# Performance work log

Hardware: AMD Instinct MI355X
Metric: run time of the kernel (lower is better)

The kernel has to match this reference:

```python
import jax, jax.numpy as jnp
import numpy as np

N, E = 65536, 524288
IN_DIM, HID_DIM, OUT_DIM = 1024, 512, 256


def setup_inputs() -> dict:
    key = jax.random.key(0)
    k1, k2, k3, k4, k5, k6 = jax.random.split(key, 6)
    h = jax.random.normal(k1, (N, IN_DIM), dtype=jnp.float32)
    src = jax.random.randint(k2, (E,), 0, N, dtype=jnp.int64)
    dst = jax.random.randint(k3, (E,), 0, N, dtype=jnp.int64)
    # Glorot-uniform weights as in DGL GraphConv
    lim1 = float(np.sqrt(6.0 / (IN_DIM + HID_DIM)))
    lim2 = float(np.sqrt(6.0 / (HID_DIM + OUT_DIM)))
    W1 = jax.random.uniform(k4, (IN_DIM, HID_DIM), jnp.float32, -lim1, lim1)
    W2 = jax.random.uniform(k5, (HID_DIM, OUT_DIM), jnp.float32, -lim2, lim2)
    b1 = jnp.zeros((HID_DIM,), jnp.float32)
    b2 = jnp.zeros((OUT_DIM,), jnp.float32)
    return {"h": h, "W1": W1, "b1": b1, "W2": W2, "b2": b2, "src": src, "dst": dst}


def _graph_conv(x, W, b, src, dst, inv_sqrt_dout, inv_sqrt_din):
    # DGL GraphConv, norm='both': D_in^{-1/2} A D_out^{-1/2} X W + b
    # Apply dense transform first (in_dim >= out_dim path in DGL) -- same math.
    x = x * inv_sqrt_dout[:, None]
    x = x @ W  # [N, out]
    agg = jax.ops.segment_sum(x[src], dst, num_segments=x.shape[0])  # scatter-add over edges
    return agg * inv_sqrt_din[:, None] + b


def reference(h, W1, b1, W2, b2, src, dst):
    n = h.shape[0]
    ones = jnp.ones((src.shape[0],), h.dtype)
    deg_out = jnp.maximum(jax.ops.segment_sum(ones, src, num_segments=n), 1.0)
    deg_in = jnp.maximum(jax.ops.segment_sum(ones, dst, num_segments=n), 1.0)
    inv_sqrt_dout = jax.lax.rsqrt(deg_out)
    inv_sqrt_din = jax.lax.rsqrt(deg_in)
    x = _graph_conv(h, W1, b1, src, dst, inv_sqrt_dout, inv_sqrt_din)
    x = jax.nn.elu(x)  # act; dropout p=0 -> identity
    out = _graph_conv(x, W2, b2, src, dst, inv_sqrt_dout, inv_sqrt_din)
    return out  # last_act = Identity
```

## Files before the change

kernel.cpp:

```cpp
#include <hip/hip_runtime.h>
#include <hip/hip_bf16.h>

#define IN_DIM 1024
#define HID 512
#define OUTD 256

typedef __attribute__((ext_vector_type(8))) short short8;
typedef __attribute__((ext_vector_type(4))) float f32x4;
typedef __attribute__((ext_vector_type(8))) unsigned short ushort8e;
typedef __attribute__((ext_vector_type(4))) unsigned int uint4e;


__device__ inline unsigned short f2bf(float f) {
    union { float f; unsigned u; } v; v.f = f;
    unsigned r = (v.u + 0x7FFF + ((v.u >> 16) & 1)) >> 16;
    return (unsigned short)r;
}

__device__ inline float bf2f(unsigned short u) {
    union { unsigned u; float f; } v; v.u = ((unsigned)u) << 16; return v.f;
}

__device__ inline unsigned pk2(float a, float b) {
    unsigned ua = __float_as_uint(a) + 0x8000u;
    unsigned ub = __float_as_uint(b) + 0x8000u;
#if __has_builtin(__builtin_amdgcn_perm)
    return __builtin_amdgcn_perm(ub, ua, 0x07060302u);
#else
    return (ua >> 16) | (ub & 0xFFFF0000u);
#endif
}

__device__ inline void gload16(const void* g, void* l) {
    __builtin_amdgcn_global_load_lds(
        (const __attribute__((address_space(1))) void*)g,
        (__attribute__((address_space(3))) void*)l, 16, 0, 0);
}


__global__ void deg_kernel(const int* __restrict__ src, const int* __restrict__ dst,
                           int* __restrict__ dego, int* __restrict__ degi, int E) {
    int i = blockIdx.x * blockDim.x + threadIdx.x;
    if (i < E) {
        atomicAdd(&dego[src[i]], 1);
        atomicAdd(&degi[dst[i]], 1);
    }
}

__global__ void invsqrt_kernel(const int* __restrict__ dego, const int* __restrict__ degi,
                               float* __restrict__ iso, float* __restrict__ isi, int n) {
    int i = blockIdx.x * blockDim.x + threadIdx.x;
    if (i < n) {
        iso[i] = rsqrtf(fmaxf((float)dego[i], 1.0f));
        isi[i] = rsqrtf(fmaxf((float)degi[i], 1.0f));
    }
}


__global__ __launch_bounds__(256) void scan_block(const int* __restrict__ deg,
                                                  int* __restrict__ excl,
                                                  int* __restrict__ partials) {
    __shared__ int tmp[256];
    int tid = threadIdx.x;
    int i = blockIdx.x * 256 + tid;
    int v = deg[i];
    tmp[tid] = v;
    __syncthreads();
    #pragma unroll
    for (int off = 1; off < 256; off <<= 1) {
        int t = (tid >= off) ? tmp[tid - off] : 0;
        __syncthreads();
        tmp[tid] += t;
        __syncthreads();
    }
    excl[i] = tmp[tid] - v;
    if (tid == 255) partials[blockIdx.x] = tmp[255];
}

__global__ __launch_bounds__(256) void scan_partials(int* __restrict__ partials) {
    __shared__ int tmp[256];
    int tid = threadIdx.x;
    int v = partials[tid];
    tmp[tid] = v;
    __syncthreads();
    #pragma unroll
    for (int off = 1; off < 256; off <<= 1) {
        int t = (tid >= off) ? tmp[tid - off] : 0;
        __syncthreads();
        tmp[tid] += t;
        __syncthreads();
    }
    partials[tid] = tmp[tid] - v;
}

__global__ __launch_bounds__(256) void scan_add(const int* __restrict__ excl,
                                                const int* __restrict__ partials,
                                                const int* __restrict__ deg,
                                                int* __restrict__ row_start,
                                                int* __restrict__ cursor, int n) {
    int i = blockIdx.x * 256 + threadIdx.x;
    int v = excl[i] + partials[blockIdx.x];
    row_start[i] = v;
    cursor[i] = v;
    if (i == n - 1) row_start[n] = v + deg[i];
}

__global__ void csr_fill(const int* __restrict__ src, const int* __restrict__ dst,
                         int* __restrict__ cursor, int* __restrict__ eidx, int E) {
    int e = blockIdx.x * blockDim.x + threadIdx.x;
    if (e < E) {
        int pos = atomicAdd(&cursor[dst[e]], 1);
        eidx[pos] = src[e];
    }
}


__global__ __launch_bounds__(256) void transpose_cvt_tiled(
    const float* __restrict__ W, unsigned short* __restrict__ Wt, int K, int N)
{
    __shared__ unsigned short tile[32][33];
    const int tx = threadIdx.x & 31;
    const int ty = threadIdx.x >> 5;
    const int n0 = blockIdx.x * 32;
    const int k0 = blockIdx.y * 32;

    #pragma unroll
    for (int j = 0; j < 4; ++j) {
        int k = ty + j * 8;
        tile[k][tx] = f2bf(W[(size_t)(k0 + k) * N + n0 + tx]);
    }
    __syncthreads();
    #pragma unroll
    for (int j = 0; j < 4; ++j) {
        int n = ty + j * 8;
        Wt[(size_t)(n0 + n) * K + k0 + tx] = tile[tx][n];
    }
}


#define NXCD 8

__global__ __launch_bounds__(256, 4) void gemm1_f32lds(
    const float* __restrict__ A, const unsigned short* __restrict__ Bt,
    unsigned short* __restrict__ Cb, int M)
{
    constexpr int K  = IN_DIM;
    constexpr int NC = HID;
    __shared__ float          As[128 * 36];
    __shared__ unsigned short Bs[128][32];

    const int tid  = threadIdx.x;
    const int lane = tid & 63;
    const int wave = tid >> 6;
    const int wr = wave >> 1, wc = wave & 1;
    const int lrow = lane & 15;
    const int lkg  = lane >> 4;

    const int per = gridDim.x / NXCD;
    const int newlin = (blockIdx.x % NXCD) * per + blockIdx.x / NXCD;
    const int ncb = NC / 128;
    const int m0 = (newlin / ncb) * 128;
    const int n0 = (newlin % ncb) * 128;

    char* AsB = (char*)&As[0];
    char* BsB = (char*)&Bs[0][0];

    int arow[5], aq[5];
    #pragma unroll
    for (int i = 0; i < 5; ++i) {
        int s = i * 256 + wave * 64 + lane;
        int r = s / 9;
        int q = s - r * 9;
        arow[i] = r;
        aq[i] = (q == 8) ? 0 : q;
    }
    int brow[2], bq[2];
    #pragma unroll
    for (int i = 0; i < 2; ++i) {
        int s = i * 256 + wave * 64 + lane;
        brow[i] = s >> 2;
        bq[i] = (s & 3) ^ ((s >> 3) & 3);
    }

    const int rslotB = (lkg ^ ((lrow >> 1) & 3)) * 8;

    f32x4 acc[4][4] = {};

    for (int kt = 0; kt < K / 32; ++kt) {
        const int k0 = kt * 32;

        #pragma unroll
        for (int i = 0; i < 4; ++i)
            gload16(A + (size_t)(m0 + arow[i]) * K + k0 + aq[i] * 4,
                    AsB + (i * 256 + wave * 64) * 16);
        if (wave < 2)
            gload16(A + (size_t)(m0 + arow[4]) * K + k0 + aq[4] * 4,
                    AsB + (4 * 256 + wave * 64) * 16);
        #pragma unroll
        for (int i = 0; i < 2; ++i)
            gload16(Bt + (size_t)(n0 + brow[i]) * K + k0 + bq[i] * 8,
                    BsB + (i * 256 + wave * 64) * 16);

        __syncthreads();

        short8 af[4], bfr[4];
        #pragma unroll
        for (int mi = 0; mi < 4; ++mi) {
            const int row = wr * 64 + mi * 16 + lrow;
            const char* rb = AsB + row * 144 + lkg * 32;
            f32x4 a0 = *reinterpret_cast<const f32x4*>(rb);
            f32x4 a1 = *reinterpret_cast<const f32x4*>(rb + 16);
            uint4e u;
            u[0] = pk2(a0[0], a0[1]); u[1] = pk2(a0[2], a0[3]);
            u[2] = pk2(a1[0], a1[1]); u[3] = pk2(a1[2], a1[3]);
            af[mi] = *reinterpret_cast<short8*>(&u);
        }
        #pragma unroll
        for (int ni = 0; ni < 4; ++ni)
            bfr[ni] = *reinterpret_cast<const short8*>(&Bs[wc * 64 + ni * 16 + lrow][rslotB]);

        #pragma unroll
        for (int mi = 0; mi < 4; ++mi)
            #pragma unroll
            for (int ni = 0; ni < 4; ++ni)
                acc[mi][ni] = __builtin_amdgcn_mfma_f32_16x16x32_bf16(
                    af[mi], bfr[ni], acc[mi][ni], 0, 0, 0);

        __syncthreads();
    }

    #pragma unroll
    for (int mi = 0; mi < 4; ++mi)
        #pragma unroll
        for (int ni = 0; ni < 4; ++ni)
            #pragma unroll
            for (int r = 0; r < 4; ++r)
                Cb[(size_t)(m0 + wr * 64 + mi * 16 + lkg * 4 + r) * NC
                   + (n0 + wc * 64 + ni * 16 + lrow)] = f2bf(acc[mi][ni][r]);
}


#define TM 128
#define TN 128
#define TK 64

__global__ __launch_bounds__(256) void gemm2_bf16(
    const unsigned short* __restrict__ Ab, const unsigned short* __restrict__ Bt,
    unsigned short* __restrict__ Cb, int M, int K, int Nc)
{
    __shared__ unsigned short As[2][TM][TK];
    __shared__ unsigned short Bs[2][TN][TK];

    const int tid  = threadIdx.x;
    const int lane = tid & 63;
    const int wave = tid >> 6;
    const int wr = wave >> 1, wc = wave & 1;
    const int lrow = lane & 15;
    const int lkg  = lane >> 4;

    const int per = gridDim.x / NXCD;
    const int newlin = (blockIdx.x % NXCD) * per + blockIdx.x / NXCD;
    const int ncb = Nc / TN;
    const int m0 = (newlin / ncb) * TM;
    const int n0 = (newlin % ncb) * TN;

    int srow[4], sq[4];
    #pragma unroll
    for (int i = 0; i < 4; ++i) {
        int s = i * 256 + wave * 64 + lane;
        srow[i] = s >> 3;
        sq[i] = (s & 7) ^ ((s >> 3) & 7);
    }

    char* AsB = (char*)&As[0][0][0];
    char* BsB = (char*)&Bs[0][0][0];

    auto stageOp = [&](const unsigned short* G, int rc0, int kt, char* opBase, int buf) {
        const int k0 = kt * TK;
        #pragma unroll
        for (int i = 0; i < 4; ++i)
            gload16(G + (size_t)(rc0 + srow[i]) * K + k0 + sq[i] * 8,
                    opBase + buf * 16384 + (i * 256 + wave * 64) * 16);
    };

    f32x4 acc[4][4] = {};

    stageOp(Bt, n0, 0, BsB, 0);
    stageOp(Ab, m0, 0, AsB, 0);
    __syncthreads();

    const int nk = K / TK;
    for (int kt = 0; kt < nk; ++kt) {
        const int cur = kt & 1, nxt = cur ^ 1;

        if (kt + 1 < nk) {
            stageOp(Bt, n0, kt + 1, BsB, nxt);
            stageOp(Ab, m0, kt + 1, AsB, nxt);
        }

        #pragma unroll
        for (int ks = 0; ks < 2; ++ks) {
            short8 af[4], bfr[4];
            #pragma unroll
            for (int mi = 0; mi < 4; ++mi) {
                const int row = wr * 64 + mi * 16 + lrow;
                const int qp = (ks * 4 + lkg) ^ (lrow & 7);
                af[mi] = *reinterpret_cast<const short8*>(&As[cur][row][qp * 8]);
            }
            #pragma unroll
            for (int ni = 0; ni < 4; ++ni) {
                const int row = wc * 64 + ni * 16 + lrow;
                const int qp = (ks * 4 + lkg) ^ (lrow & 7);
                bfr[ni] = *reinterpret_cast<const short8*>(&Bs[cur][row][qp * 8]);
            }
            #pragma unroll
            for (int mi = 0; mi < 4; ++mi)
                #pragma unroll
                for (int ni = 0; ni < 4; ++ni)
                    acc[mi][ni] = __builtin_amdgcn_mfma_f32_16x16x32_bf16(
                        af[mi], bfr[ni], acc[mi][ni], 0, 0, 0);
        }

        __syncthreads();
    }

    #pragma unroll
    for (int mi = 0; mi < 4; ++mi)
        #pragma unroll
        for (int ni = 0; ni < 4; ++ni)
            #pragma unroll
            for (int r = 0; r < 4; ++r)
                Cb[(size_t)(m0 + wr * 64 + mi * 16 + lkg * 4 + r) * Nc
                   + (n0 + wc * 64 + ni * 16 + lrow)] = f2bf(acc[mi][ni][r]);
}


template<int DIM, int LANES, bool LAYER1>
__global__ __launch_bounds__(256) void aggregate(
    const int* __restrict__ row_start, const int* __restrict__ eidx,
    const unsigned short* __restrict__ Xb, const float* __restrict__ isi,
    const float* __restrict__ iso, const float* __restrict__ bias,
    unsigned short* __restrict__ out_bf, float* __restrict__ out_f)
{
    constexpr int F = DIM / LANES;
    constexpr int NPB = 256 / LANES;
    const int node = blockIdx.x * NPB + (threadIdx.x / LANES);
    const int lane = threadIdx.x % LANES;

    const int beg = row_start[node];
    const int end = row_start[node + 1];
    const unsigned short* base = Xb + lane * F;

    float acc[F] = {};
    int e = beg;
    for (; e + 3 < end; e += 4) {
        int i0 = eidx[e], i1 = eidx[e + 1], i2 = eidx[e + 2], i3 = eidx[e + 3];
        float s0 = 1.f, s1 = 1.f, s2 = 1.f, s3 = 1.f;
        if (LAYER1) { s0 = iso[i0]; s1 = iso[i1]; s2 = iso[i2]; s3 = iso[i3]; }
        ushort8e v0 = *reinterpret_cast<const ushort8e*>(base + (size_t)i0 * DIM);
        ushort8e v1 = *reinterpret_cast<const ushort8e*>(base + (size_t)i1 * DIM);
        ushort8e v2 = *reinterpret_cast<const ushort8e*>(base + (size_t)i2 * DIM);
        ushort8e v3 = *reinterpret_cast<const ushort8e*>(base + (size_t)i3 * DIM);
        #pragma unroll
        for (int f = 0; f < F; ++f) {
            if (LAYER1) {
                acc[f] = fmaf(s0, bf2f(v0[f]), acc[f]);
                acc[f] = fmaf(s1, bf2f(v1[f]), acc[f]);
                acc[f] = fmaf(s2, bf2f(v2[f]), acc[f]);
                acc[f] = fmaf(s3, bf2f(v3[f]), acc[f]);
            } else {
                acc[f] += bf2f(v0[f]); acc[f] += bf2f(v1[f]);
                acc[f] += bf2f(v2[f]); acc[f] += bf2f(v3[f]);
            }
        }
    }
    for (; e < end; ++e) {
        int i0 = eidx[e];
        float s0 = LAYER1 ? iso[i0] : 1.f;
        ushort8e v0 = *reinterpret_cast<const ushort8e*>(base + (size_t)i0 * DIM);
        #pragma unroll
        for (int f = 0; f < F; ++f)
            acc[f] = LAYER1 ? fmaf(s0, bf2f(v0[f]), acc[f]) : acc[f] + bf2f(v0[f]);
    }

    const float si = isi[node];
    float bv[F];
    #pragma unroll
    for (int q = 0; q < F / 4; ++q)
        *reinterpret_cast<float4*>(&bv[q * 4]) =
            *reinterpret_cast<const float4*>(bias + lane * F + q * 4);

    if (LAYER1) {
        const float so = iso[node];
        short8 o;
        #pragma unroll
        for (int f = 0; f < F; ++f) {
            float v = acc[f] * si + bv[f];
            v = v > 0.f ? v : expm1f(v);
            o[f] = (short)f2bf(v * so);
        }
        *reinterpret_cast<short8*>(out_bf + (size_t)node * DIM + lane * F) = o;
    } else {
        #pragma unroll
        for (int q = 0; q < F / 4; ++q) {
            float4 v = make_float4(acc[q * 4 + 0] * si + bv[q * 4 + 0],
                                   acc[q * 4 + 1] * si + bv[q * 4 + 1],
                                   acc[q * 4 + 2] * si + bv[q * 4 + 2],
                                   acc[q * 4 + 3] * si + bv[q * 4 + 3]);
            *reinterpret_cast<float4*>(out_f + (size_t)node * DIM + lane * F + q * 4) = v;
        }
    }
}


extern "C" void kernel_launch(void* const* d_in, const int* in_sizes, int n_in,
                              void* d_out, int out_size, void* d_ws, size_t ws_size,
                              hipStream_t stream) {
    const float* h  = (const float*)d_in[0];
    const float* W1 = (const float*)d_in[1];
    const float* b1 = (const float*)d_in[2];
    const float* W2 = (const float*)d_in[3];
    const float* b2 = (const float*)d_in[4];
    const int*   src = (const int*)d_in[5];
    const int*   dst = (const int*)d_in[6];

    const int N = in_sizes[0] / IN_DIM;
    const int E = in_sizes[5];
    float* out = (float*)d_out;

    int* dego      = (int*)d_ws;
    int* degi      = dego + N;
    int* excl      = degi + N;
    int* partials  = excl + N;
    int* row_start = partials + 256;
    int* cursor    = row_start + N + 64;
    int* eidx      = cursor + N;
    float* iso     = (float*)(eidx + E);
    float* isi     = iso + N;
    unsigned short* W1t = (unsigned short*)(isi + N);
    unsigned short* W2t = W1t + (size_t)IN_DIM * HID;
    unsigned short* X1b = W2t + (size_t)HID * OUTD;
    unsigned short* X2b = X1b;
    unsigned short* R2h = X1b + (size_t)N * HID;

    hipMemsetAsync(dego, 0, sizeof(int) * (size_t)2 * N, stream);

    deg_kernel<<<(E + 255) / 256, 256, 0, stream>>>(src, dst, dego, degi, E);
    invsqrt_kernel<<<(N + 255) / 256, 256, 0, stream>>>(dego, degi, iso, isi, N);

    scan_block<<<N / 256, 256, 0, stream>>>(degi, excl, partials);
    scan_partials<<<1, 256, 0, stream>>>(partials);
    scan_add<<<N / 256, 256, 0, stream>>>(excl, partials, degi, row_start, cursor, N);
    csr_fill<<<(E + 255) / 256, 256, 0, stream>>>(src, dst, cursor, eidx, E);

    {
        dim3 g1(HID / 32, IN_DIM / 32);
        transpose_cvt_tiled<<<g1, 256, 0, stream>>>(W1, W1t, IN_DIM, HID);
        dim3 g2(OUTD / 32, HID / 32);
        transpose_cvt_tiled<<<g2, 256, 0, stream>>>(W2, W2t, HID, OUTD);
    }

    gemm1_f32lds<<<(N / 128) * (HID / 128), 256, 0, stream>>>(h, W1t, X1b, N);
    aggregate<HID, 64, true><<<N / 4, 256, 0, stream>>>(
        row_start, eidx, X1b, isi, iso, b1, R2h, nullptr);

    gemm2_bf16<<<(N / TM) * (OUTD / TN), 256, 0, stream>>>(
        R2h, W2t, X2b, N, HID, OUTD);
    aggregate<OUTD, 32, false><<<N / 8, 256, 0, stream>>>(
        row_start, eidx, X2b, isi, iso, b2, nullptr, out);
}
```

Baseline: 392.1 us.

## Double-buffer LDS tiles in gemm1 with prefetch two stages ahead

Converts the first GEMM's single-buffered LDS tiles into two buffers. The tile for the iteration after next is issued asynchronously while the current one is consumed, with manual vmcnt waits and raw s_barrier calls replacing __syncthreads. The goal is to hide global-to-LDS load latency behind MFMA work. LDS use roughly doubles, which may lower occupancy below the launch-bounds target of 4 blocks per CU, and the hand-counted vmcnt values are fragile.

After: 406.4 us. 3.7% more time.

```diff
diff --git a/kernel.cpp b/kernel.cpp
--- a/kernel.cpp
+++ b/kernel.cpp
@@ -146,8 +146,8 @@
 {
     constexpr int K  = IN_DIM;
     constexpr int NC = HID;
-    __shared__ float          As[128 * 36];
-    __shared__ unsigned short Bs[128][32];
+    __shared__ float          As[2][128 * 36];
+    __shared__ unsigned short Bs[2][128][32];
 
     const int tid  = threadIdx.x;
     const int lane = tid & 63;
@@ -162,8 +162,8 @@
     const int m0 = (newlin / ncb) * 128;
     const int n0 = (newlin % ncb) * 128;
 
-    char* AsB = (char*)&As[0];
-    char* BsB = (char*)&Bs[0][0];
+    char* AsB = (char*)&As[0][0];
+    char* BsB = (char*)&Bs[0][0][0];
 
     int arow[5], aq[5];
     #pragma unroll
@@ -182,32 +182,44 @@
         bq[i] = (s & 3) ^ ((s >> 3) & 3);
     }
 
-    const int rslotB = (lkg ^ ((lrow >> 1) & 3)) * 8;
-
-    f32x4 acc[4][4] = {};
-
-    for (int kt = 0; kt < K / 32; ++kt) {
+    auto stage = [&](int kt, int buf) {
         const int k0 = kt * 32;
-
         #pragma unroll
         for (int i = 0; i < 4; ++i)
             gload16(A + (size_t)(m0 + arow[i]) * K + k0 + aq[i] * 4,
-                    AsB + (i * 256 + wave * 64) * 16);
+                    AsB + buf * 18432 + (i * 256 + wave * 64) * 16);
         if (wave < 2)
             gload16(A + (size_t)(m0 + arow[4]) * K + k0 + aq[4] * 4,
-                    AsB + (4 * 256 + wave * 64) * 16);
+                    AsB + buf * 18432 + (4 * 256 + wave * 64) * 16);
         #pragma unroll
         for (int i = 0; i < 2; ++i)
             gload16(Bt + (size_t)(n0 + brow[i]) * K + k0 + bq[i] * 8,
-                    BsB + (i * 256 + wave * 64) * 16);
-
-        __syncthreads();
+                    BsB + buf * 8192 + (i * 256 + wave * 64) * 16);
+    };
+    auto waitS = [&]() {
+        if (wave < 2) asm volatile("s_waitcnt vmcnt(7)" ::: "memory");
+        else          asm volatile("s_waitcnt vmcnt(6)" ::: "memory");
+    };
+
+    const int rslotB = (lkg ^ ((lrow >> 1) & 3)) * 8;
+
+    f32x4 acc[4][4] = {};
+
+    stage(0, 0);
+    stage(1, 1);
+    waitS();
+    __builtin_amdgcn_sched_barrier(0);
+    __builtin_amdgcn_s_barrier();
+
+    const int nk = K / 32;
+    for (int kt = 0; kt < nk; ++kt) {
+        const int cur = kt & 1;
 
         short8 af[4], bfr[4];
         #pragma unroll
         for (int mi = 0; mi < 4; ++mi) {
             const int row = wr * 64 + mi * 16 + lrow;
-            const char* rb = AsB + row * 144 + lkg * 32;
+            const char* rb = AsB + cur * 18432 + row * 144 + lkg * 32;
             f32x4 a0 = *reinterpret_cast<const f32x4*>(rb);
             f32x4 a1 = *reinterpret_cast<const f32x4*>(rb + 16);
             uint4e u;
@@ -217,7 +229,8 @@
         }
         #pragma unroll
         for (int ni = 0; ni < 4; ++ni)
-            bfr[ni] = *reinterpret_cast<const short8*>(&Bs[wc * 64 + ni * 16 + lrow][rslotB]);
+            bfr[ni] = *reinterpret_cast<const short8*>(
+                &Bs[cur][wc * 64 + ni * 16 + lrow][rslotB]);
 
         #pragma unroll
         for (int mi = 0; mi < 4; ++mi)
@@ -226,7 +239,16 @@
                 acc[mi][ni] = __builtin_amdgcn_mfma_f32_16x16x32_bf16(
                     af[mi], bfr[ni], acc[mi][ni], 0, 0, 0);
 
-        __syncthreads();
+        __builtin_amdgcn_s_barrier();
+
+        if (kt + 2 < nk) {
+            stage(kt + 2, cur);
+            waitS();
+        } else if (kt + 1 < nk) {
+            asm volatile("s_waitcnt vmcnt(0)" ::: "memory");
+        }
+        __builtin_amdgcn_sched_barrier(0);
+        __builtin_amdgcn_s_barrier();
     }
 
     #pragma unroll
```

## Prescale and convert input to bf16 before GEMM1, drop per-edge scaling

Applied to the files above, without the earlier changes.

Adds a standalone pass that multiplies h by the out-degree normalisation and converts it to bf16. GEMM1 can then stream bf16 tiles directly instead of converting fp32 in LDS. The layer-1 aggregation no longer gathers per-edge source scales. This trades an extra full read/write pass over the large input for smaller GEMM loads and a simpler gather loop.

Measured after the change: 437.5 us. +11.6%, slower.

```diff
diff --git a/kernel.cpp b/kernel.cpp
--- a/kernel.cpp
+++ b/kernel.cpp
@@ -8,7 +8,6 @@
 typedef __attribute__((ext_vector_type(8))) short short8;
 typedef __attribute__((ext_vector_type(4))) float f32x4;
 typedef __attribute__((ext_vector_type(8))) unsigned short ushort8e;
-typedef __attribute__((ext_vector_type(4))) unsigned int uint4e;
 
 
 __device__ inline unsigned short f2bf(float f) {
@@ -19,16 +18,6 @@
 
 __device__ inline float bf2f(unsigned short u) {
     union { unsigned u; float f; } v; v.u = ((unsigned)u) << 16; return v.f;
-}
-
-__device__ inline unsigned pk2(float a, float b) {
-    unsigned ua = __float_as_uint(a) + 0x8000u;
-    unsigned ub = __float_as_uint(b) + 0x8000u;
-#if __has_builtin(__builtin_amdgcn_perm)
-    return __builtin_amdgcn_perm(ub, ua, 0x07060302u);
-#else
-    return (ua >> 16) | (ub & 0xFFFF0000u);
-#endif
 }
 
 __device__ inline void gload16(const void* g, void* l) {
@@ -115,6 +104,24 @@
 }
 
 
+__global__ __launch_bounds__(256) void scale_cvt(
+    const float* __restrict__ x, const float* __restrict__ rs,
+    unsigned short* __restrict__ y, int logK, size_t total)
+{
+    const size_t stride = (size_t)gridDim.x * 256 * 8;
+    for (size_t i = ((size_t)blockIdx.x * 256 + threadIdx.x) * 8; i < total; i += stride) {
+        float s = rs[i >> logK];
+        float4 a = *reinterpret_cast<const float4*>(x + i);
+        float4 b = *reinterpret_cast<const float4*>(x + i + 4);
+        short8 o;
+        o[0] = (short)f2bf(a.x * s); o[1] = (short)f2bf(a.y * s);
+        o[2] = (short)f2bf(a.z * s); o[3] = (short)f2bf(a.w * s);
+        o[4] = (short)f2bf(b.x * s); o[5] = (short)f2bf(b.y * s);
+        o[6] = (short)f2bf(b.z * s); o[7] = (short)f2bf(b.w * s);
+        *reinterpret_cast<short8*>(y + i) = o;
+    }
+}
+
 __global__ __launch_bounds__(256) void transpose_cvt_tiled(
     const float* __restrict__ W, unsigned short* __restrict__ Wt, int K, int N)
 {
@@ -140,13 +147,11 @@
 
 #define NXCD 8
 
-__global__ __launch_bounds__(256, 4) void gemm1_f32lds(
-    const float* __restrict__ A, const unsigned short* __restrict__ Bt,
-    unsigned short* __restrict__ Cb, int M)
+__global__ __launch_bounds__(256) void gemm1_bf16(
+    const unsigned short* __restrict__ A, const unsigned short* __restrict__ Bt,
+    unsigned short* __restrict__ Cb, int M, int K, int Nc)
 {
-    constexpr int K  = IN_DIM;
-    constexpr int NC = HID;
-    __shared__ float          As[128 * 36];
+    __shared__ unsigned short As[128][32];
     __shared__ unsigned short Bs[128][32];
 
     const int tid  = threadIdx.x;
@@ -158,66 +163,42 @@
 
     const int per = gridDim.x / NXCD;
     const int newlin = (blockIdx.x % NXCD) * per + blockIdx.x / NXCD;
-    const int ncb = NC / 128;
+    const int ncb = Nc / 128;
     const int m0 = (newlin / ncb) * 128;
     const int n0 = (newlin % ncb) * 128;
 
-    char* AsB = (char*)&As[0];
+    const int s0 = wave * 64 + lane;
+    const int s1 = s0 + 256;
+    const int r0 = s0 >> 2, q0 = (s0 & 3) ^ ((s0 >> 3) & 3);
+    const int r1 = s1 >> 2, q1 = (s1 & 3) ^ ((s1 >> 3) & 3);
+
+    char* AsB = (char*)&As[0][0];
     char* BsB = (char*)&Bs[0][0];
-
-    int arow[5], aq[5];
-    #pragma unroll
-    for (int i = 0; i < 5; ++i) {
-        int s = i * 256 + wave * 64 + lane;
-        int r = s / 9;
-        int q = s - r * 9;
-        arow[i] = r;
-        aq[i] = (q == 8) ? 0 : q;
-    }
-    int brow[2], bq[2];
-    #pragma unroll
-    for (int i = 0; i < 2; ++i) {
-        int s = i * 256 + wave * 64 + lane;
-        brow[i] = s >> 2;
-        bq[i] = (s & 3) ^ ((s >> 3) & 3);
-    }
-
-    const int rslotB = (lkg ^ ((lrow >> 1) & 3)) * 8;
+    void* ldsA0 = AsB + wave * 1024;
+    void* ldsA1 = AsB + 4096 + wave * 1024;
+    void* ldsB0 = BsB + wave * 1024;
+    void* ldsB1 = BsB + 4096 + wave * 1024;
+
+    const int rslot = (lkg ^ ((lrow >> 1) & 3)) * 8;
 
     f32x4 acc[4][4] = {};
 
-    for (int kt = 0; kt < K / 32; ++kt) {
+    const int nk = K / 32;
+    for (int kt = 0; kt < nk; ++kt) {
         const int k0 = kt * 32;
-
-        #pragma unroll
-        for (int i = 0; i < 4; ++i)
-            gload16(A + (size_t)(m0 + arow[i]) * K + k0 + aq[i] * 4,
-                    AsB + (i * 256 + wave * 64) * 16);
-        if (wave < 2)
-            gload16(A + (size_t)(m0 + arow[4]) * K + k0 + aq[4] * 4,
-                    AsB + (4 * 256 + wave * 64) * 16);
-        #pragma unroll
-        for (int i = 0; i < 2; ++i)
-            gload16(Bt + (size_t)(n0 + brow[i]) * K + k0 + bq[i] * 8,
-                    BsB + (i * 256 + wave * 64) * 16);
-
+        gload16(A  + (size_t)(m0 + r0) * K + k0 + q0 * 8, ldsA0);
+        gload16(A  + (size_t)(m0 + r1) * K + k0 + q1 * 8, ldsA1);
+        gload16(Bt + (size_t)(n0 + r0) * K + k0 + q0 * 8, ldsB0);
+        gload16(Bt + (size_t)(n0 + r1) * K + k0 + q1 * 8, ldsB1);
         __syncthreads();
 
         short8 af[4], bfr[4];
         #pragma unroll
-        for (int mi = 0; mi < 4; ++mi) {
-            const int row = wr * 64 + mi * 16 + lrow;
-            const char* rb = AsB + row * 144 + lkg * 32;
-            f32x4 a0 = *reinterpret_cast<const f32x4*>(rb);
-            f32x4 a1 = *reinterpret_cast<const f32x4*>(rb + 16);
-            uint4e u;
-            u[0] = pk2(a0[0], a0[1]); u[1] = pk2(a0[2], a0[3]);
-            u[2] = pk2(a1[0], a1[1]); u[3] = pk2(a1[2], a1[3]);
-            af[mi] = *reinterpret_cast<short8*>(&u);
-        }
+        for (int mi = 0; mi < 4; ++mi)
+            af[mi] = *reinterpret_cast<const short8*>(&As[wr * 64 + mi * 16 + lrow][rslot]);
         #pragma unroll
         for (int ni = 0; ni < 4; ++ni)
-            bfr[ni] = *reinterpret_cast<const short8*>(&Bs[wc * 64 + ni * 16 + lrow][rslotB]);
+            bfr[ni] = *reinterpret_cast<const short8*>(&Bs[wc * 64 + ni * 16 + lrow][rslot]);
 
         #pragma unroll
         for (int mi = 0; mi < 4; ++mi)
@@ -235,7 +216,7 @@
         for (int ni = 0; ni < 4; ++ni)
             #pragma unroll
             for (int r = 0; r < 4; ++r)
-                Cb[(size_t)(m0 + wr * 64 + mi * 16 + lkg * 4 + r) * NC
+                Cb[(size_t)(m0 + wr * 64 + mi * 16 + lkg * 4 + r) * Nc
                    + (n0 + wc * 64 + ni * 16 + lrow)] = f2bf(acc[mi][ni][r]);
 }
 
@@ -335,7 +316,7 @@
 }
 
 
-template<int DIM, int LANES, bool LAYER1>
+template<int DIM, int LANES, bool ELU>
 __global__ __launch_bounds__(256) void aggregate(
     const int* __restrict__ row_start, const int* __restrict__ eidx,
     const unsigned short* __restrict__ Xb, const float* __restrict__ isi,
@@ -355,32 +336,20 @@
     int e = beg;
     for (; e + 3 < end; e += 4) {
         int i0 = eidx[e], i1 = eidx[e + 1], i2 = eidx[e + 2], i3 = eidx[e + 3];
-        float s0 = 1.f, s1 = 1.f, s2 = 1.f, s3 = 1.f;
-        if (LAYER1) { s0 = iso[i0]; s1 = iso[i1]; s2 = iso[i2]; s3 = iso[i3]; }
         ushort8e v0 = *reinterpret_cast<const ushort8e*>(base + (size_t)i0 * DIM);
         ushort8e v1 = *reinterpret_cast<const ushort8e*>(base + (size_t)i1 * DIM);
         ushort8e v2 = *reinterpret_cast<const ushort8e*>(base + (size_t)i2 * DIM);
         ushort8e v3 = *reinterpret_cast<const ushort8e*>(base + (size_t)i3 * DIM);
         #pragma unroll
         for (int f = 0; f < F; ++f) {
-            if (LAYER1) {
-                acc[f] = fmaf(s0, bf2f(v0[f]), acc[f]);
-                acc[f] = fmaf(s1, bf2f(v1[f]), acc[f]);
-                acc[f] = fmaf(s2, bf2f(v2[f]), acc[f]);
-                acc[f] = fmaf(s3, bf2f(v3[f]), acc[f]);
-            } else {
-                acc[f] += bf2f(v0[f]); acc[f] += bf2f(v1[f]);
-                acc[f] += bf2f(v2[f]); acc[f] += bf2f(v3[f]);
-            }
+            acc[f] += bf2f(v0[f]); acc[f] += bf2f(v1[f]);
+            acc[f] += bf2f(v2[f]); acc[f] += bf2f(v3[f]);
         }
     }
     for (; e < end; ++e) {
-        int i0 = eidx[e];
-        float s0 = LAYER1 ? iso[i0] : 1.f;
-        ushort8e v0 = *reinterpret_cast<const ushort8e*>(base + (size_t)i0 * DIM);
-        #pragma unroll
-        for (int f = 0; f < F; ++f)
-            acc[f] = LAYER1 ? fmaf(s0, bf2f(v0[f]), acc[f]) : acc[f] + bf2f(v0[f]);
+        ushort8e v0 = *reinterpret_cast<const ushort8e*>(base + (size_t)eidx[e] * DIM);
+        #pragma unroll
+        for (int f = 0; f < F; ++f) acc[f] += bf2f(v0[f]);
     }
 
     const float si = isi[node];
@@ -390,7 +359,7 @@
         *reinterpret_cast<float4*>(&bv[q * 4]) =
             *reinterpret_cast<const float4*>(bias + lane * F + q * 4);
 
-    if (LAYER1) {
+    if (ELU) {
         const float so = iso[node];
         short8 o;
         #pragma unroll
@@ -439,7 +408,8 @@
     float* isi     = iso + N;
     unsigned short* W1t = (unsigned short*)(isi + N);
     unsigned short* W2t = W1t + (size_t)IN_DIM * HID;
-    unsigned short* X1b = W2t + (size_t)HID * OUTD;
+    unsigned short* hb  = W2t + (size_t)HID * OUTD;
+    unsigned short* X1b = hb + (size_t)N * IN_DIM;
     unsigned short* X2b = X1b;
     unsigned short* R2h = X1b + (size_t)N * HID;
 
@@ -453,6 +423,7 @@
     scan_add<<<N / 256, 256, 0, stream>>>(excl, partials, degi, row_start, cursor, N);
     csr_fill<<<(E + 255) / 256, 256, 0, stream>>>(src, dst, cursor, eidx, E);
 
+    scale_cvt<<<2048, 256, 0, stream>>>(h, iso, hb, 10, (size_t)N * IN_DIM);
     {
         dim3 g1(HID / 32, IN_DIM / 32);
         transpose_cvt_tiled<<<g1, 256, 0, stream>>>(W1, W1t, IN_DIM, HID);
@@ -460,7 +431,8 @@
         transpose_cvt_tiled<<<g2, 256, 0, stream>>>(W2, W2t, HID, OUTD);
     }
 
-    gemm1_f32lds<<<(N / 128) * (HID / 128), 256, 0, stream>>>(h, W1t, X1b, N);
+    gemm1_bf16<<<(N / 128) * (HID / 128), 256, 0, stream>>>(
+        hb, W1t, X1b, N, IN_DIM, HID);
     aggregate<HID, 64, true><<<N / 4, 256, 0, stream>>>(
         row_start, eidx, X1b, isi, iso, b1, R2h, nullptr);
 
```
